# Kernel tuning notes

Hardware: AMD Instinct MI355X
Metric: run time of the kernel (lower is better)

## Reference

```python
import jax, jax.numpy as jnp
import numpy as np

# Model dims (match init_kwargs)
INPUT_CAPS = 2048
INPUT_DIM = 16
OUTPUT_CAPS = 16
OUTPUT_DIM = 16
D = OUTPUT_CAPS * OUTPUT_DIM  # 256
BATCH = 64


def setup_inputs() -> dict:
    key = jax.random.key(0)
    k1, k2 = jax.random.split(key)
    caps_output = jax.random.normal(k1, (BATCH, INPUT_CAPS, INPUT_DIM), dtype=jnp.float32)
    stdv = 1.0 / np.sqrt(INPUT_CAPS)
    weights = jax.random.uniform(k2, (INPUT_CAPS, INPUT_DIM, D),
                                 minval=-stdv, maxval=stdv, dtype=jnp.float32)
    return {"caps_output": caps_output, "weights": weights}


def reference(caps_output, weights):
    # u_predict[b,c,:] = caps_output[b,c,:] @ weights[c]  -> [B, IC, D]
    u = jnp.einsum('bci,cio->bco', caps_output, weights)
    # Gram matrix C = A^T A  -> [B, D, D], symmetric PSD (real eigenvalues)
    C = jnp.einsum('bcd,bce->bde', u, u)
    # Top eigenpair. Original code uses np.linalg.eig per batch on CPU and
    # selects the largest eigenvalue; C is symmetric so eigh is the faithful
    # (and efficient) form. eigh returns ascending order -> take last column.
    e_vals, e_vecs = jnp.linalg.eigh(C)
    v = e_vecs[:, :, -1]  # [B, D] dominant eigenvector
    # Fix eigenvector sign deterministically (largest-|component| positive)
    idx = jnp.argmax(jnp.abs(v), axis=1)
    sgn = jnp.sign(jnp.take_along_axis(v, idx[:, None], axis=1))
    v = v * sgn
    return v.reshape(BATCH, OUTPUT_CAPS, OUTPUT_DIM)
```

## Files before the change

kernel.cpp:

```cpp
#include <hip/hip_runtime.h>

#define NB  64
#define IC  2048
#define ID  16
#define DD  256
#define DDSQ 65536
#define PB  (DDSQ * NB)
#define NSQ 11
#define NPI 7

typedef __attribute__((ext_vector_type(8))) short          s16x8;
typedef __attribute__((ext_vector_type(4))) float          f32x4;
typedef __attribute__((ext_vector_type(4))) unsigned short us4;
typedef __attribute__((ext_vector_type(8))) unsigned short us8;

__device__ __forceinline__ unsigned short f2b(float f) {
    union { float f; unsigned u; } c; c.f = f;
    const unsigned u = c.u + 0x7FFFu + ((c.u >> 16) & 1u);
    return (unsigned short)(u >> 16);
}
__device__ __forceinline__ float b2f(unsigned short h) {
    union { unsigned u; float f; } c; c.u = ((unsigned)h) << 16;
    return c.f;
}
__device__ __forceinline__ unsigned f2pk(float f) {
    const unsigned short h = f2b(f);
    const unsigned short l = f2b(f - b2f(h));
    return ((unsigned)h << 16) | (unsigned)l;
}

__global__ __launch_bounds__(256, 4) void u_kernel(const float* __restrict__ caps,
                                                   const float* __restrict__ W,
                                                   unsigned* __restrict__ U) {
    const int c = blockIdx.x;
    const int t = threadIdx.x;
    __shared__ float xsT[ID][64];
    {
        const int b = t >> 2, q = (t & 3) * 4;
        const float4 x4 = *(const float4*)&caps[((size_t)b * IC + c) * ID + q];
        xsT[q + 0][b] = x4.x; xsT[q + 1][b] = x4.y;
        xsT[q + 2][b] = x4.z; xsT[q + 3][b] = x4.w;
    }
    __syncthreads();
    float a[64];
#pragma unroll
    for (int b = 0; b < 64; ++b) a[b] = 0.f;
#pragma unroll
    for (int i = 0; i < ID; ++i) {
        const float wi = W[((size_t)c * ID + i) * DD + t];
#pragma unroll
        for (int g = 0; g < 16; ++g) {
            const float4 x = *(const float4*)&xsT[i][g * 4];
            a[g * 4 + 0] = fmaf(x.x, wi, a[g * 4 + 0]);
            a[g * 4 + 1] = fmaf(x.y, wi, a[g * 4 + 1]);
            a[g * 4 + 2] = fmaf(x.z, wi, a[g * 4 + 2]);
            a[g * 4 + 3] = fmaf(x.w, wi, a[g * 4 + 3]);
        }
    }
#pragma unroll
    for (int b = 0; b < 64; ++b)
        U[((size_t)b * IC + c) * DD + t] = f2pk(a[b]);
}

__global__ __launch_bounds__(256, 2)
void cmb_kernel(const unsigned* __restrict__ Up,
                unsigned short* __restrict__ Ch, unsigned short* __restrict__ Cl,
                float* __restrict__ Sc) {
    const int id   = blockIdx.x;
    const int bb   = id & 63;
    const int tile = id >> 6;
    const int tr = tile >> 2, tc = tile & 3;
    const int d0 = tr * 128, e0 = tc * 64;
    const int t    = threadIdx.x;
    const int lane = t & 63, wid = t >> 6;
    const int wm = wid >> 1, wn = wid & 1;
    const int fr = lane & 15, kg = lane >> 4;
    const int sl8 = lane & 7, qg = lane >> 3;
    const size_t mb = (size_t)bb * DDSQ;

    __shared__ unsigned short Ah[128][40];
    __shared__ unsigned short Al[128][40];
    __shared__ unsigned short Bh[64][40];
    __shared__ unsigned short Bl[64][40];
    __shared__ float red[256];

    const f32x4 z4 = {0.f, 0.f, 0.f, 0.f};
    f32x4 acc[4][2];
#pragma unroll
    for (int m = 0; m < 4; ++m)
#pragma unroll
        for (int n = 0; n < 2; ++n) acc[m][n] = z4;

    const unsigned* Ub = Up + (size_t)bb * IC * DD;
    unsigned va[4][4], vb[2][4];
    auto loadU = [&](int kb) {
#pragma unroll
        for (int s = 0; s < 4; ++s) {
            const int row = wid * 8 + sl8 + 32 * s;
#pragma unroll
            for (int j = 0; j < 4; ++j)
                va[s][j] = Ub[(size_t)(kb + 4 * qg + j) * DD + d0 + row];
        }
#pragma unroll
        for (int s = 0; s < 2; ++s) {
            const int row = wid * 8 + sl8 + 32 * s;
#pragma unroll
            for (int j = 0; j < 4; ++j)
                vb[s][j] = Ub[(size_t)(kb + 4 * qg + j) * DD + e0 + row];
        }
    };

    loadU(0);
    for (int kb = 0; kb < IC; kb += 32) {
        __syncthreads();
#pragma unroll
        for (int s = 0; s < 4; ++s) {
            const int row = wid * 8 + sl8 + 32 * s;
            us4 h, l;
#pragma unroll
            for (int j = 0; j < 4; ++j) {
                h[j] = (unsigned short)(va[s][j] >> 16);
                l[j] = (unsigned short)(va[s][j] & 0xFFFFu);
            }
            *(us4*)&Ah[row][4 * qg] = h;
            *(us4*)&Al[row][4 * qg] = l;
        }
#pragma unroll
        for (int s = 0; s < 2; ++s) {
            const int row = wid * 8 + sl8 + 32 * s;
            us4 h, l;
#pragma unroll
            for (int j = 0; j < 4; ++j) {
                h[j] = (unsigned short)(vb[s][j] >> 16);
                l[j] = (unsigned short)(vb[s][j] & 0xFFFFu);
            }
            *(us4*)&Bh[row][4 * qg] = h;
            *(us4*)&Bl[row][4 * qg] = l;
        }
        __syncthreads();
        if (kb + 32 < IC) loadU(kb + 32);
        s16x8 ah[4], al[4], bh[2], bl[2];
#pragma unroll
        for (int m = 0; m < 4; ++m) {
            const int r = wm * 64 + m * 16 + fr;
            ah[m] = *(const s16x8*)&Ah[r][kg * 8];
            al[m] = *(const s16x8*)&Al[r][kg * 8];
        }
#pragma unroll
        for (int n = 0; n < 2; ++n) {
            const int r = wn * 32 + n * 16 + fr;
            bh[n] = *(const s16x8*)&Bh[r][kg * 8];
            bl[n] = *(const s16x8*)&Bl[r][kg * 8];
        }
#pragma unroll
        for (int m = 0; m < 4; ++m)
#pragma unroll
            for (int n = 0; n < 2; ++n) {
                acc[m][n] = __builtin_amdgcn_mfma_f32_16x16x32_bf16(ah[m], bh[n], acc[m][n], 0, 0, 0);
                acc[m][n] = __builtin_amdgcn_mfma_f32_16x16x32_bf16(ah[m], bl[n], acc[m][n], 0, 0, 0);
                acc[m][n] = __builtin_amdgcn_mfma_f32_16x16x32_bf16(al[m], bh[n], acc[m][n], 0, 0, 0);
            }
    }

    float ts = 0.f;
    const int row_l = wm * 64 + (lane >> 4) * 4;
    const int col_l = wn * 32 + fr;
#pragma unroll
    for (int m = 0; m < 4; ++m)
#pragma unroll
        for (int n = 0; n < 2; ++n)
#pragma unroll
            for (int r = 0; r < 4; ++r) {
                const int gr = d0 + row_l + m * 16 + r;
                const int gc = e0 + col_l + n * 16;
                const float e = acc[m][n][r];
                const unsigned short h = f2b(e);
                const unsigned short l = f2b(e - b2f(h));
                const size_t o = mb + (size_t)gr * DD + gc;
                Ch[o] = h; Cl[o] = l;
                if (gr == gc) ts += e;
            }
    if ((tc >> 1) == tr) {
        red[t] = ts;
        __syncthreads();
        for (int s2 = 128; s2 > 0; s2 >>= 1) {
            if (t < s2) red[t] += red[t + s2];
            __syncthreads();
        }
        if (t == 0) atomicAdd(&Sc[bb], red[0]);
    }
}

__global__ __launch_bounds__(256, 4)
void sqm_kernel(const unsigned short* __restrict__ Dh, const unsigned short* __restrict__ Dl,
                unsigned short* __restrict__ Eh, unsigned short* __restrict__ El,
                const float* __restrict__ s_in, float* __restrict__ s_out) {
    const int id   = blockIdx.x;
    const int bb   = id & 63;
    const int tile = id >> 6;
    const int tr = tile >> 2, tc = tile & 3;
    const int d0 = tr * 64, e0 = tc * 64;
    const int t    = threadIdx.x;
    const int lane = t & 63, wid = t >> 6;
    const int wm = wid >> 1, wn = wid & 1;
    const int fr = lane & 15, kg = lane >> 4;
    const size_t mb = (size_t)bb * DDSQ;

    __shared__ unsigned short Ah[64][40];
    __shared__ unsigned short Al[64][40];
    __shared__ unsigned short Bh[64][40];
    __shared__ unsigned short Bl[64][40];
    __shared__ float red[256];

    const f32x4 z4 = {0.f, 0.f, 0.f, 0.f};
    f32x4 acc[2][2];
#pragma unroll
    for (int m = 0; m < 2; ++m)
#pragma unroll
        for (int n = 0; n < 2; ++n) acc[m][n] = z4;

    const float s   = s_in[bb];
    const float inv = 1.f / (s * s);
    const int row = t >> 2, q = t & 3;

    for (int kb = 0; kb < DD; kb += 32) {
        const size_t ga = mb + (size_t)(d0 + row) * DD + kb + q * 8;
        const size_t gb = mb + (size_t)(e0 + row) * DD + kb + q * 8;
        const int4 rah = *(const int4*)&Dh[ga];
        const int4 ral = *(const int4*)&Dl[ga];
        const int4 rbh = *(const int4*)&Dh[gb];
        const int4 rbl = *(const int4*)&Dl[gb];
        __syncthreads();
        *(int4*)&Ah[row][q * 8] = rah;
        *(int4*)&Al[row][q * 8] = ral;
        *(int4*)&Bh[row][q * 8] = rbh;
        *(int4*)&Bl[row][q * 8] = rbl;
        __syncthreads();

        s16x8 ah[2], al[2], bh[2], bl[2];
#pragma unroll
        for (int m = 0; m < 2; ++m) {
            const int r = wm * 32 + m * 16 + fr;
            ah[m] = *(const s16x8*)&Ah[r][kg * 8];
            al[m] = *(const s16x8*)&Al[r][kg * 8];
        }
#pragma unroll
        for (int n = 0; n < 2; ++n) {
            const int r = wn * 32 + n * 16 + fr;
            bh[n] = *(const s16x8*)&Bh[r][kg * 8];
            bl[n] = *(const s16x8*)&Bl[r][kg * 8];
        }
#pragma unroll
        for (int m = 0; m < 2; ++m)
#pragma unroll
            for (int n = 0; n < 2; ++n) {
                acc[m][n] = __builtin_amdgcn_mfma_f32_16x16x32_bf16(ah[m], bh[n], acc[m][n], 0, 0, 0);
                acc[m][n] = __builtin_amdgcn_mfma_f32_16x16x32_bf16(ah[m], bl[n], acc[m][n], 0, 0, 0);
                acc[m][n] = __builtin_amdgcn_mfma_f32_16x16x32_bf16(al[m], bh[n], acc[m][n], 0, 0, 0);
            }
    }

    float ts = 0.f;
    const int row_l = wm * 32 + (lane >> 4) * 4;
    const int col_l = wn * 32 + fr;
#pragma unroll
    for (int m = 0; m < 2; ++m)
#pragma unroll
        for (int n = 0; n < 2; ++n)
#pragma unroll
            for (int r = 0; r < 4; ++r) {
                const int gr = d0 + row_l + m * 16 + r;
                const int gc = e0 + col_l + n * 16;
                const float e = acc[m][n][r] * inv;
                const unsigned short h = f2b(e);
                const unsigned short l = f2b(e - b2f(h));
                const size_t o = mb + (size_t)gr * DD + gc;
                Eh[o] = h; El[o] = l;
                if (gr == gc) ts += e;
            }
    if (tr == tc) {
        red[t] = ts;
        __syncthreads();
        for (int s2 = 128; s2 > 0; s2 >>= 1) {
            if (t < s2) red[t] += red[t + s2];
            __syncthreads();
        }
        if (t == 0) atomicAdd(&s_out[bb], red[0]);
    }
}

__global__ __launch_bounds__(256, 2) void finish_kernel(const unsigned short* __restrict__ Dh,
                                                        const unsigned short* __restrict__ Dl,
                                                        float* __restrict__ out) {
    const int b = blockIdx.x, t = threadIdx.x;
    const size_t mb = (size_t)b * DDSQ;
    __shared__ float vs[DD];
    __shared__ float red[DD];
    __shared__ int   ridx[DD];
    red[t] = b2f(Dh[mb + (size_t)t * DD + t]) + b2f(Dl[mb + (size_t)t * DD + t]);
    ridx[t] = t;
    __syncthreads();
    for (int s = 128; s > 0; s >>= 1) {
        if (t < s && red[t + s] > red[t]) { red[t] = red[t + s]; ridx[t] = ridx[t + s]; }
        __syncthreads();
    }
    const int jmax0 = ridx[0];
    __syncthreads();
    float v = b2f(Dh[mb + (size_t)jmax0 * DD + t]) + b2f(Dl[mb + (size_t)jmax0 * DD + t]);
    for (int it = 0; it < NPI; ++it) {
        vs[t] = v;
        __syncthreads();
        float a = 0.f;
        const unsigned short* rh = Dh + mb + (size_t)t * DD;
        const unsigned short* rl = Dl + mb + (size_t)t * DD;
#pragma unroll 4
        for (int j = 0; j < DD; j += 8) {
            const us8 h8 = *(const us8*)&rh[j];
            const us8 l8 = *(const us8*)&rl[j];
            a = fmaf(b2f(h8[0]) + b2f(l8[0]), vs[j + 0], a);
            a = fmaf(b2f(h8[1]) + b2f(l8[1]), vs[j + 1], a);
            a = fmaf(b2f(h8[2]) + b2f(l8[2]), vs[j + 2], a);
            a = fmaf(b2f(h8[3]) + b2f(l8[3]), vs[j + 3], a);
            a = fmaf(b2f(h8[4]) + b2f(l8[4]), vs[j + 4], a);
            a = fmaf(b2f(h8[5]) + b2f(l8[5]), vs[j + 5], a);
            a = fmaf(b2f(h8[6]) + b2f(l8[6]), vs[j + 6], a);
            a = fmaf(b2f(h8[7]) + b2f(l8[7]), vs[j + 7], a);
        }
        __syncthreads();
        v = a;
    }
    vs[t] = v;
    red[t] = v * v;
    __syncthreads();
    for (int s = 128; s > 0; s >>= 1) {
        if (t < s) red[t] += red[t + s];
        __syncthreads();
    }
    const float nrm = sqrtf(red[0]);
    __syncthreads();
    red[t] = fabsf(v);
    ridx[t] = t;
    __syncthreads();
    for (int s = 128; s > 0; s >>= 1) {
        if (t < s && red[t + s] > red[t]) { red[t] = red[t + s]; ridx[t] = ridx[t + s]; }
        __syncthreads();
    }
    const float sgn = (vs[ridx[0]] < 0.f) ? -1.f : 1.f;
    out[(size_t)b * DD + t] = sgn * v / nrm;
}

extern "C" void kernel_launch(void* const* d_in, const int* in_sizes, int n_in,
                              void* d_out, int out_size, void* d_ws, size_t ws_size,
                              hipStream_t stream) {
    const float* caps = (const float*)d_in[0];
    const float* W    = (const float*)d_in[1];
    float* out = (float*)d_out;
    float* ws  = (float*)d_ws;

    unsigned* Up = (unsigned*)ws;
    unsigned short* Xh = (unsigned short*)(ws + (size_t)8 * PB);
    unsigned short* Xl = Xh + (size_t)NB * DDSQ;
    unsigned short* Yh = (unsigned short*)(ws + (size_t)9 * PB);
    unsigned short* Yl = Yh + (size_t)NB * DDSQ;
    float* Sc = ws + (size_t)10 * PB;

    hipMemsetAsync(Sc, 0, 2048 * sizeof(float), stream);

    u_kernel<<<IC, 256, 0, stream>>>(caps, W, Up);
    cmb_kernel<<<512, 256, 0, stream>>>(Up, Xh, Xl, Sc);

    unsigned short* ph = Xh; unsigned short* pl = Xl;
    unsigned short* qh = Yh; unsigned short* ql = Yl;
    for (int it = 0; it < NSQ; ++it) {
        sqm_kernel<<<1024, 256, 0, stream>>>(ph, pl, qh, ql,
                                             Sc + it * 64, Sc + (it + 1) * 64);
        unsigned short* t1 = ph; ph = qh; qh = t1;
        unsigned short* t2 = pl; pl = ql; ql = t2;
    }

    finish_kernel<<<NB, 256, 0, stream>>>(ph, pl, out);
}
```

Measured before the change: 382.2 us.

## Exploit symmetry in repeated squaring: compute upper-triangular tiles and mirror

The squared matrix is symmetric, so the kernel now computes only the 10 upper-triangular 64x64 tiles per batch instead of 16 and writes each off-diagonal tile to its transposed position as well. The grid shrinks from 1024 to 640 blocks. The K-loop also stages 64-wide K chunks in shared memory, which halves the number of barrier pairs but enlarges the LDS footprint. The mirrored stores are strided 8-byte writes, which add scattered memory traffic.

```diff
diff --git a/kernel.cpp b/kernel.cpp
--- a/kernel.cpp
+++ b/kernel.cpp
@@ -198,7 +198,11 @@
     const int id   = blockIdx.x;
     const int bb   = id & 63;
     const int tile = id >> 6;
-    const int tr = tile >> 2, tc = tile & 3;
+    int tr, tc;
+    if (tile < 4)      { tr = 0; tc = tile; }
+    else if (tile < 7) { tr = 1; tc = tile - 3; }
+    else if (tile < 9) { tr = 2; tc = tile - 5; }
+    else               { tr = 3; tc = 3; }
     const int d0 = tr * 64, e0 = tc * 64;
     const int t    = threadIdx.x;
     const int lane = t & 63, wid = t >> 6;
@@ -206,10 +210,10 @@
     const int fr = lane & 15, kg = lane >> 4;
     const size_t mb = (size_t)bb * DDSQ;
 
-    __shared__ unsigned short Ah[64][40];
-    __shared__ unsigned short Al[64][40];
-    __shared__ unsigned short Bh[64][40];
-    __shared__ unsigned short Bl[64][40];
+    __shared__ unsigned short Ah[64][72];
+    __shared__ unsigned short Al[64][72];
+    __shared__ unsigned short Bh[64][72];
+    __shared__ unsigned short Bl[64][72];
     __shared__ float red[256];
 
     const f32x4 z4 = {0.f, 0.f, 0.f, 0.f};
@@ -223,61 +227,82 @@
     const float inv = 1.f / (s * s);
     const int row = t >> 2, q = t & 3;
 
-    for (int kb = 0; kb < DD; kb += 32) {
+    for (int kb = 0; kb < DD; kb += 64) {
         const size_t ga = mb + (size_t)(d0 + row) * DD + kb + q * 8;
         const size_t gb = mb + (size_t)(e0 + row) * DD + kb + q * 8;
-        const int4 rah = *(const int4*)&Dh[ga];
-        const int4 ral = *(const int4*)&Dl[ga];
-        const int4 rbh = *(const int4*)&Dh[gb];
-        const int4 rbl = *(const int4*)&Dl[gb];
-        __syncthreads();
-        *(int4*)&Ah[row][q * 8] = rah;
-        *(int4*)&Al[row][q * 8] = ral;
-        *(int4*)&Bh[row][q * 8] = rbh;
-        *(int4*)&Bl[row][q * 8] = rbl;
-        __syncthreads();
-
-        s16x8 ah[2], al[2], bh[2], bl[2];
-#pragma unroll
-        for (int m = 0; m < 2; ++m) {
-            const int r = wm * 32 + m * 16 + fr;
-            ah[m] = *(const s16x8*)&Ah[r][kg * 8];
-            al[m] = *(const s16x8*)&Al[r][kg * 8];
-        }
-#pragma unroll
-        for (int n = 0; n < 2; ++n) {
-            const int r = wn * 32 + n * 16 + fr;
-            bh[n] = *(const s16x8*)&Bh[r][kg * 8];
-            bl[n] = *(const s16x8*)&Bl[r][kg * 8];
-        }
-#pragma unroll
-        for (int m = 0; m < 2; ++m)
+        const int4 rah0 = *(const int4*)&Dh[ga];
+        const int4 rah1 = *(const int4*)&Dh[ga + 32];
+        const int4 ral0 = *(const int4*)&Dl[ga];
+        const int4 ral1 = *(const int4*)&Dl[ga + 32];
+        const int4 rbh0 = *(const int4*)&Dh[gb];
+        const int4 rbh1 = *(const int4*)&Dh[gb + 32];
+        const int4 rbl0 = *(const int4*)&Dl[gb];
+        const int4 rbl1 = *(const int4*)&Dl[gb + 32];
+        __syncthreads();
+        *(int4*)&Ah[row][q * 8]      = rah0;
+        *(int4*)&Ah[row][q * 8 + 32] = rah1;
+        *(int4*)&Al[row][q * 8]      = ral0;
+        *(int4*)&Al[row][q * 8 + 32] = ral1;
+        *(int4*)&Bh[row][q * 8]      = rbh0;
+        *(int4*)&Bh[row][q * 8 + 32] = rbh1;
+        *(int4*)&Bl[row][q * 8]      = rbl0;
+        *(int4*)&Bl[row][q * 8 + 32] = rbl1;
+        __syncthreads();
+
+#pragma unroll
+        for (int h = 0; h < 2; ++h) {
+            const int ko = kg * 8 + 32 * h;
+            s16x8 ah[2], al[2], bh[2], bl[2];
+#pragma unroll
+            for (int m = 0; m < 2; ++m) {
+                const int r = wm * 32 + m * 16 + fr;
+                ah[m] = *(const s16x8*)&Ah[r][ko];
+                al[m] = *(const s16x8*)&Al[r][ko];
+            }
 #pragma unroll
             for (int n = 0; n < 2; ++n) {
-                acc[m][n] = __builtin_amdgcn_mfma_f32_16x16x32_bf16(ah[m], bh[n], acc[m][n], 0, 0, 0);
-                acc[m][n] = __builtin_amdgcn_mfma_f32_16x16x32_bf16(ah[m], bl[n], acc[m][n], 0, 0, 0);
-                acc[m][n] = __builtin_amdgcn_mfma_f32_16x16x32_bf16(al[m], bh[n], acc[m][n], 0, 0, 0);
-            }
+                const int r = wn * 32 + n * 16 + fr;
+                bh[n] = *(const s16x8*)&Bh[r][ko];
+                bl[n] = *(const s16x8*)&Bl[r][ko];
+            }
+#pragma unroll
+            for (int m = 0; m < 2; ++m)
+#pragma unroll
+                for (int n = 0; n < 2; ++n) {
+                    acc[m][n] = __builtin_amdgcn_mfma_f32_16x16x32_bf16(ah[m], bh[n], acc[m][n], 0, 0, 0);
+                    acc[m][n] = __builtin_amdgcn_mfma_f32_16x16x32_bf16(ah[m], bl[n], acc[m][n], 0, 0, 0);
+                    acc[m][n] = __builtin_amdgcn_mfma_f32_16x16x32_bf16(al[m], bh[n], acc[m][n], 0, 0, 0);
+                }
+        }
     }
 
     float ts = 0.f;
     const int row_l = wm * 32 + (lane >> 4) * 4;
     const int col_l = wn * 32 + fr;
+    const bool mir = (tr != tc);
 #pragma unroll
     for (int m = 0; m < 2; ++m)
 #pragma unroll
-        for (int n = 0; n < 2; ++n)
+        for (int n = 0; n < 2; ++n) {
+            const int gr0 = d0 + row_l + m * 16;
+            const int gc  = e0 + col_l + n * 16;
+            us4 h4, l4;
 #pragma unroll
             for (int r = 0; r < 4; ++r) {
-                const int gr = d0 + row_l + m * 16 + r;
-                const int gc = e0 + col_l + n * 16;
                 const float e = acc[m][n][r] * inv;
                 const unsigned short h = f2b(e);
                 const unsigned short l = f2b(e - b2f(h));
-                const size_t o = mb + (size_t)gr * DD + gc;
+                const size_t o = mb + (size_t)(gr0 + r) * DD + gc;
                 Eh[o] = h; El[o] = l;
-                if (gr == gc) ts += e;
-            }
+                h4[r] = h; l4[r] = l;
+                if (gr0 + r == gc) ts += e;
+            }
+            if (mir) {
+                const size_t o2 = mb + (size_t)gc * DD + gr0;
+                *(us4*)&Eh[o2] = h4;
+                *(us4*)&El[o2] = l4;
+            }
+        }
     if (tr == tc) {
         red[t] = ts;
         __syncthreads();
@@ -372,8 +397,8 @@
     unsigned short* ph = Xh; unsigned short* pl = Xl;
     unsigned short* qh = Yh; unsigned short* ql = Yl;
     for (int it = 0; it < NSQ; ++it) {
-        sqm_kernel<<<1024, 256, 0, stream>>>(ph, pl, qh, ql,
-                                             Sc + it * 64, Sc + (it + 1) * 64);
+        sqm_kernel<<<640, 256, 0, stream>>>(ph, pl, qh, ql,
+                                            Sc + it * 64, Sc + (it + 1) * 64);
         unsigned short* t1 = ph; ph = qh; qh = t1;
         unsigned short* t2 = pl; pl = ql; ql = t2;
     }
```

Measured after the change: 371.4 us. 2.8% less time.
